# Kernel optimization log

Hardware: AMD Instinct MI355X
Metric: run time of the kernel (lower is better)

The kernel has to match this reference:

```python
import jax, jax.numpy as jnp
import numpy as np

H = 8192  # hidden_size == input_size
NNZ = 1_000_000
B = 128
T = 64


def _spmm(rows, cols, values, x, out_dim):
    # y[r, :] += v * x[c, :] for each nnz (r, c, v); matches coalesced COO spmm
    gathered = values[:, None] * x[cols]          # [nnz, B]
    return jax.ops.segment_sum(gathered, rows, num_segments=out_dim)  # [out_dim, B]


def setup_inputs() -> dict:
    key = jax.random.key(0)
    ks = jax.random.split(key, 5)
    x = jax.random.normal(ks[0], (B, T, H), dtype=jnp.float32)
    ih_indices = jax.random.randint(ks[1], (2, NNZ), 0, H, dtype=jnp.int32)
    hh_indices = jax.random.randint(ks[2], (2, NNZ), 0, H, dtype=jnp.int32)
    # scale so tanh pre-activations stay in a reasonable range (~122 nnz/row)
    ih_values = jax.random.normal(ks[3], (NNZ,), dtype=jnp.float32) * 0.05
    hh_values = jax.random.normal(ks[4], (NNZ,), dtype=jnp.float32) * 0.05
    bias_ih = jnp.zeros((H, 1), dtype=jnp.float32)
    bias_hh = jnp.zeros((H, 1), dtype=jnp.float32)
    return {
        "x": x,
        "ih_indices": ih_indices,
        "ih_values": ih_values,
        "hh_indices": hh_indices,
        "hh_values": hh_values,
        "bias_ih": bias_ih,
        "bias_hh": bias_hh,
    }


def reference(x, ih_indices, ih_values, hh_indices, hh_values, bias_ih, bias_hh):
    # x: (batch, seq, features) -> (T, F, B) as in torch permute(1, 2, 0)
    xs = jnp.transpose(x, (1, 2, 0))  # [T, H, B]
    ih_r, ih_c = ih_indices[0], ih_indices[1]
    hh_r, hh_c = hh_indices[0], hh_indices[1]

    def step(h, x_t):
        pre = (_spmm(ih_r, ih_c, ih_values, x_t, H) + bias_ih
               + _spmm(hh_r, hh_c, hh_values, h, H) + bias_hh)
        h_new = jnp.tanh(pre)
        return h_new, h_new

    h0 = jnp.zeros((H, x.shape[0]), dtype=x.dtype)
    _, out = jax.lax.scan(step, h0, xs)  # out: [T, H, B]
    return jnp.transpose(out, (2, 0, 1))  # [B, T, H] (batch_first)
```

## Files before the change

### kernel.cpp

```cpp
#include <hip/hip_runtime.h>
#include <cstdint>
#include <cstddef>
#include <cstring>

#define H 8192
#define NNZ 1000000
#define B 128
#define T 64

typedef unsigned int u32;
typedef u32 u32x2 __attribute__((ext_vector_type(2)));

__device__ inline float bf_lo(u32 w) { return __uint_as_float(w << 16); }
__device__ inline float bf_hi(u32 w) { return __uint_as_float(w & 0xffff0000u); }
__device__ inline unsigned short f2bf(float f) {
    u32 v = __float_as_uint(f);
    v += 0x7fffu + ((v >> 16) & 1u);
    return (unsigned short)(v >> 16);
}
__device__ inline u32 pack_bf16(float a, float b) {
    return (u32)f2bf(a) | ((u32)f2bf(b) << 16);
}
__device__ inline float fast_tanh(float x) {
    float e = __expf(2.0f * x);
    return 1.0f - 2.0f / (e + 1.0f);
}

__global__ void hist_kernel(const int* __restrict__ rows, int nnz, int* __restrict__ count) {
    int j = blockIdx.x * blockDim.x + threadIdx.x;
    if (j < nnz) atomicAdd(&count[rows[j]], 1);
}

__global__ void scan_kernel(const int* __restrict__ cnt0, int* __restrict__ rp0, int* __restrict__ cur0,
                            const int* __restrict__ cnt1, int* __restrict__ rp1, int* __restrict__ cur1) {
    const int* cnt = (blockIdx.x == 0) ? cnt0 : cnt1;
    int* rp  = (blockIdx.x == 0) ? rp0 : rp1;
    int* cur = (blockIdx.x == 0) ? cur0 : cur1;
    __shared__ int buf[1024];
    __shared__ int carry;
    int tid = threadIdx.x;
    if (tid == 0) carry = 0;
    __syncthreads();
    for (int base = 0; base < H; base += 1024) {
        int v = cnt[base + tid];
        buf[tid] = v;
        __syncthreads();
        for (int off = 1; off < 1024; off <<= 1) {
            int t = (tid >= off) ? buf[tid - off] : 0;
            __syncthreads();
            buf[tid] += t;
            __syncthreads();
        }
        int incl = buf[tid];
        int excl = incl - v;
        int c = carry;
        rp[base + tid]  = c + excl;
        cur[base + tid] = c + excl;
        __syncthreads();
        if (tid == 1023) carry = c + incl;
        __syncthreads();
    }
    if (tid == 0) rp[H] = carry;
}

__global__ void scatter_kernel(const int* __restrict__ rows, const int* __restrict__ cols,
                               const float* __restrict__ vals, int nnz,
                               int* __restrict__ cursor, int2* __restrict__ opair) {
    int j = blockIdx.x * blockDim.x + threadIdx.x;
    if (j < nnz) {
        int r = rows[j];
        int p = atomicAdd(&cursor[r], 1);
        opair[p] = make_int2(cols[j], __float_as_int(vals[j]));
    }
}

__global__ void transpose_bf16_kernel(const float* __restrict__ src, u32* __restrict__ dst) {
    __shared__ float tile[32][33];
    int c0 = blockIdx.x * 32;
    int r0 = blockIdx.y * 32;
    int x = threadIdx.x, y = threadIdx.y;
    #pragma unroll
    for (int i = y; i < 32; i += 8) {
        tile[i][x] = src[(size_t)(r0 + i) * (T * H) + (c0 + x)];
    }
    __syncthreads();
    int tid = y * 32 + x;
    #pragma unroll
    for (int idx = tid; idx < 32 * 16; idx += 256) {
        int row = idx >> 4, w = idx & 15;
        u32 word = pack_bf16(tile[2 * w][row], tile[2 * w + 1][row]);
        dst[(size_t)(c0 + row) * 64 + (r0 >> 1) + w] = word;
    }
}

__global__ void transpose_out_kernel(const u32* __restrict__ src, float* __restrict__ dst) {
    __shared__ u32 tile[32][33];
    int c0 = blockIdx.x * 32;
    int w0 = blockIdx.y * 32;
    int x = threadIdx.x, y = threadIdx.y;
    #pragma unroll
    for (int i = y; i < 32; i += 8) {
        tile[i][x] = src[(size_t)(c0 + i) * 64 + (w0 + x)];
    }
    __syncthreads();
    #pragma unroll
    for (int i = y; i < 64; i += 8) {
        int w = i >> 1;
        u32 word = tile[x][w];
        float val = (i & 1) ? bf_hi(word) : bf_lo(word);
        dst[(size_t)(2 * w0 + i) * (size_t)(T * H) + (c0 + x)] = val;
    }
}

__global__ void __launch_bounds__(64) ih_pre_kernel(
    const int* __restrict__ rp, const int2* __restrict__ pair,
    const u32* __restrict__ xTb, u32* __restrict__ pre,
    const float* __restrict__ bias_ih, const float* __restrict__ bias_hh) {
    int bid = blockIdx.x;
    int xcd = bid & 7;
    int i0  = bid >> 3;
    int t   = (xcd << 3) + (i0 >> 13);
    int r   = i0 & (H - 1);
    int lane = threadIdx.x;
    bool hi = lane >= 32;
    int i = lane & 31;
    const char* __restrict__ xtb = (const char*)(xTb + (size_t)t * H * 64);
    const u32 i8 = (u32)i * 8u;
    float ax = 0.f, ay = 0.f, az = 0.f, aw = 0.f;
    int s = rp[r], e = rp[r + 1];
    int j = s;
    for (; j + 16 <= e; j += 16) {
        int2 q[16];
        #pragma unroll
        for (int u = 0; u < 16; ++u) q[u] = pair[j + u];
        u32x2 g[8];
        #pragma unroll
        for (int u = 0; u < 8; ++u) {
            u32 c = (u32)(hi ? q[2 * u + 1].x : q[2 * u].x);
            g[u] = *(const u32x2*)(xtb + ((c << 8) + i8));
        }
        #pragma unroll
        for (int u = 0; u < 8; ++u) {
            float v = __int_as_float(hi ? q[2 * u + 1].y : q[2 * u].y);
            ax = fmaf(v, bf_lo(g[u].x), ax);
            ay = fmaf(v, bf_hi(g[u].x), ay);
            az = fmaf(v, bf_lo(g[u].y), az);
            aw = fmaf(v, bf_hi(g[u].y), aw);
        }
    }
    for (; j + 2 <= e; j += 2) {
        int2 q0 = pair[j], q1 = pair[j + 1];
        u32 c = (u32)(hi ? q1.x : q0.x);
        u32x2 g = *(const u32x2*)(xtb + ((c << 8) + i8));
        float v = __int_as_float(hi ? q1.y : q0.y);
        ax = fmaf(v, bf_lo(g.x), ax);
        ay = fmaf(v, bf_hi(g.x), ay);
        az = fmaf(v, bf_lo(g.y), az);
        aw = fmaf(v, bf_hi(g.y), aw);
    }
    if (j < e) {
        int2 q0 = pair[j];
        u32 c = (u32)q0.x;
        u32x2 g = *(const u32x2*)(xtb + ((c << 8) + i8));
        float v = hi ? 0.0f : __int_as_float(q0.y);
        ax = fmaf(v, bf_lo(g.x), ax);
        ay = fmaf(v, bf_hi(g.x), ay);
        az = fmaf(v, bf_lo(g.y), az);
        aw = fmaf(v, bf_hi(g.y), aw);
    }
    float tx = ax + __shfl_xor(ax, 32, 64);
    float ty = ay + __shfl_xor(ay, 32, 64);
    float tz = az + __shfl_xor(az, 32, 64);
    float tw = aw + __shfl_xor(aw, 32, 64);
    if (lane < 32) {
        float bias = bias_ih[r] + bias_hh[r];
        u32x2 pw;
        pw.x = pack_bf16(tx + bias, ty + bias);
        pw.y = pack_bf16(tz + bias, tw + bias);
        __builtin_nontemporal_store(pw, (u32x2*)(pre + ((size_t)t * H + r) * 64) + i);
    }
}

__global__ void __launch_bounds__(256) step_kernel(
    const int* __restrict__ rp, const int2* __restrict__ pair,
    const u32* __restrict__ hprev, u32* __restrict__ hout,
    const u32* __restrict__ pre_t) {
    const int tid  = threadIdx.x;
    const int wav  = tid >> 6;
    const int lane = tid & 63;
    const bool hi  = lane >= 32;
    const int i    = lane & 31;
    const u32 i8   = (u32)i * 8u;
    const int r = __builtin_amdgcn_readfirstlane(((int)blockIdx.x << 2) + wav);
    u32x2 pw = __builtin_nontemporal_load((const u32x2*)pre_t + (size_t)r * 32 + i);
    float ax = 0.f, ay = 0.f, az = 0.f, aw = 0.f;
    if (hprev) {
        const char* __restrict__ hpb = (const char*)hprev;
        int s = rp[r], e = rp[r + 1];
        int j = s;
        for (; j + 16 <= e; j += 16) {
            int2 q[16];
            #pragma unroll
            for (int u = 0; u < 16; ++u) q[u] = pair[j + u];
            u32x2 g[8];
            #pragma unroll
            for (int u = 0; u < 8; ++u) {
                u32 c = (u32)(hi ? q[2 * u + 1].x : q[2 * u].x);
                g[u] = *(const u32x2*)(hpb + ((c << 8) + i8));
            }
            #pragma unroll
            for (int u = 0; u < 8; ++u) {
                float v = __int_as_float(hi ? q[2 * u + 1].y : q[2 * u].y);
                ax = fmaf(v, bf_lo(g[u].x), ax);
                ay = fmaf(v, bf_hi(g[u].x), ay);
                az = fmaf(v, bf_lo(g[u].y), az);
                aw = fmaf(v, bf_hi(g[u].y), aw);
            }
        }
        for (; j + 2 <= e; j += 2) {
            int2 q0 = pair[j], q1 = pair[j + 1];
            u32 c = (u32)(hi ? q1.x : q0.x);
            u32x2 g = *(const u32x2*)(hpb + ((c << 8) + i8));
            float v = __int_as_float(hi ? q1.y : q0.y);
            ax = fmaf(v, bf_lo(g.x), ax);
            ay = fmaf(v, bf_hi(g.x), ay);
            az = fmaf(v, bf_lo(g.y), az);
            aw = fmaf(v, bf_hi(g.y), aw);
        }
        if (j < e) {
            int2 q0 = pair[j];
            u32 c = (u32)q0.x;
            u32x2 g = *(const u32x2*)(hpb + ((c << 8) + i8));
            float v = hi ? 0.0f : __int_as_float(q0.y);
            ax = fmaf(v, bf_lo(g.x), ax);
            ay = fmaf(v, bf_hi(g.x), ay);
            az = fmaf(v, bf_lo(g.y), az);
            aw = fmaf(v, bf_hi(g.y), aw);
        }
        ax += __shfl_xor(ax, 32, 64);
        ay += __shfl_xor(ay, 32, 64);
        az += __shfl_xor(az, 32, 64);
        aw += __shfl_xor(aw, 32, 64);
    }
    if (lane < 32) {
        float h0 = fast_tanh(ax + bf_lo(pw.x));
        float h1 = fast_tanh(ay + bf_hi(pw.x));
        float h2v = fast_tanh(az + bf_lo(pw.y));
        float h3 = fast_tanh(aw + bf_hi(pw.y));
        u32x2 hw;
        hw.x = pack_bf16(h0, h1);
        hw.y = pack_bf16(h2v, h3);
        ((u32x2*)hout)[(size_t)r * 32 + i] = hw;
    }
}

extern "C" void kernel_launch(void* const* d_in, const int* in_sizes, int n_in,
                              void* d_out, int out_size, void* d_ws, size_t ws_size,
                              hipStream_t stream) {
    const float* x        = (const float*)d_in[0];
    const int*   ih_idx   = (const int*)d_in[1];
    const float* ih_val   = (const float*)d_in[2];
    const int*   hh_idx   = (const int*)d_in[3];
    const float* hh_val   = (const float*)d_in[4];
    const float* bias_ih  = (const float*)d_in[5];
    const float* bias_hh  = (const float*)d_in[6];
    const int* ih_rows = ih_idx;
    const int* ih_cols = ih_idx + NNZ;
    const int* hh_rows = hh_idx;
    const int* hh_cols = hh_idx + NNZ;

    char* ws = (char*)d_ws;
    size_t off = 0;
    auto alloc = [&](size_t bytes) -> void* {
        void* p = ws + off;
        off += (bytes + 255) & ~(size_t)255;
        return p;
    };
    u32*   xTb     = (u32*)  alloc((size_t)T * H * 64 * 4);
    u32*   pre     = (u32*)  alloc((size_t)T * H * 64 * 4);
    u32*   outb    = (u32*)  alloc((size_t)T * H * 64 * 4);
    int2*  pair_ih = (int2*) alloc((size_t)NNZ * 8);
    int2*  pair_hh = (int2*) alloc((size_t)NNZ * 8);
    int*   rp_ih   = (int*)  alloc((size_t)(H + 1) * 4);
    int*   rp_hh   = (int*)  alloc((size_t)(H + 1) * 4);
    int*   cnt_ih  = (int*)  alloc((size_t)H * 4);
    int*   cnt_hh  = (int*)  alloc((size_t)H * 4);
    int*   cur_ih  = (int*)  alloc((size_t)H * 4);
    int*   cur_hh  = (int*)  alloc((size_t)H * 4);

    hipMemsetAsync(cnt_ih, 0, (size_t)H * 4, stream);
    hipMemsetAsync(cnt_hh, 0, (size_t)H * 4, stream);

    const int tb = 256;
    const int gb = (NNZ + tb - 1) / tb;
    hist_kernel<<<gb, tb, 0, stream>>>(ih_rows, NNZ, cnt_ih);
    hist_kernel<<<gb, tb, 0, stream>>>(hh_rows, NNZ, cnt_hh);
    scan_kernel<<<2, 1024, 0, stream>>>(cnt_ih, rp_ih, cur_ih, cnt_hh, rp_hh, cur_hh);
    scatter_kernel<<<gb, tb, 0, stream>>>(ih_rows, ih_cols, ih_val, NNZ, cur_ih, pair_ih);
    scatter_kernel<<<gb, tb, 0, stream>>>(hh_rows, hh_cols, hh_val, NNZ, cur_hh, pair_hh);

    dim3 tblk(32, 8);
    dim3 tgrid1((T * H) / 32, B / 32);
    transpose_bf16_kernel<<<tgrid1, tblk, 0, stream>>>(x, xTb);

    ih_pre_kernel<<<T * H, 64, 0, stream>>>(rp_ih, pair_ih, xTb, pre, bias_ih, bias_hh);

    step_kernel<<<H / 4, 256, 0, stream>>>(rp_hh, pair_hh, (const u32*)nullptr,
                                           outb, pre);
    for (int t = 1; t < T; ++t) {
        step_kernel<<<H / 4, 256, 0, stream>>>(rp_hh, pair_hh,
                                               outb + (size_t)(t - 1) * H * 64,
                                               outb + (size_t)t * H * 64,
                                               pre + (size_t)t * H * 64);
    }

    dim3 tgrid2((T * H) / 32, 2);
    transpose_out_kernel<<<tgrid2, tblk, 0, stream>>>(outb, (float*)d_out);
}
```

Measured before the change: 2.571 ms.

## Overlap input-projection SpMM with recurrent steps by fusing future timesteps into step kernel

```diff
diff --git a/kernel.cpp b/kernel.cpp
--- a/kernel.cpp
+++ b/kernel.cpp
@@ -26,9 +26,57 @@
     return 1.0f - 2.0f / (e + 1.0f);
 }
 
-__global__ void hist_kernel(const int* __restrict__ rows, int nnz, int* __restrict__ count) {
+__device__ inline void spmm_row(const int* __restrict__ rp, const int2* __restrict__ pair,
+                                const char* __restrict__ basep, int r, bool hi, u32 i8,
+                                float& ax, float& ay, float& az, float& aw) {
+    int s = rp[r], e = rp[r + 1];
+    int j = s;
+    for (; j + 16 <= e; j += 16) {
+        int2 q[16];
+        #pragma unroll
+        for (int u = 0; u < 16; ++u) q[u] = pair[j + u];
+        u32x2 g[8];
+        #pragma unroll
+        for (int u = 0; u < 8; ++u) {
+            u32 c = (u32)(hi ? q[2 * u + 1].x : q[2 * u].x);
+            g[u] = *(const u32x2*)(basep + ((c << 8) + i8));
+        }
+        #pragma unroll
+        for (int u = 0; u < 8; ++u) {
+            float v = __int_as_float(hi ? q[2 * u + 1].y : q[2 * u].y);
+            ax = fmaf(v, bf_lo(g[u].x), ax);
+            ay = fmaf(v, bf_hi(g[u].x), ay);
+            az = fmaf(v, bf_lo(g[u].y), az);
+            aw = fmaf(v, bf_hi(g[u].y), aw);
+        }
+    }
+    for (; j + 2 <= e; j += 2) {
+        int2 q0 = pair[j], q1 = pair[j + 1];
+        u32 c = (u32)(hi ? q1.x : q0.x);
+        u32x2 g = *(const u32x2*)(basep + ((c << 8) + i8));
+        float v = __int_as_float(hi ? q1.y : q0.y);
+        ax = fmaf(v, bf_lo(g.x), ax);
+        ay = fmaf(v, bf_hi(g.x), ay);
+        az = fmaf(v, bf_lo(g.y), az);
+        aw = fmaf(v, bf_hi(g.y), aw);
+    }
+    if (j < e) {
+        int2 q0 = pair[j];
+        u32 c = (u32)q0.x;
+        u32x2 g = *(const u32x2*)(basep + ((c << 8) + i8));
+        float v = hi ? 0.0f : __int_as_float(q0.y);
+        ax = fmaf(v, bf_lo(g.x), ax);
+        ay = fmaf(v, bf_hi(g.x), ay);
+        az = fmaf(v, bf_lo(g.y), az);
+        aw = fmaf(v, bf_hi(g.y), aw);
+    }
+}
+
+__global__ void hist2_kernel(const int* __restrict__ rows_a, const int* __restrict__ rows_b,
+                             int* __restrict__ cnt_a, int* __restrict__ cnt_b) {
     int j = blockIdx.x * blockDim.x + threadIdx.x;
-    if (j < nnz) atomicAdd(&count[rows[j]], 1);
+    if (j < NNZ) atomicAdd(&cnt_a[rows_a[j]], 1);
+    else if (j < 2 * NNZ) atomicAdd(&cnt_b[rows_b[j - NNZ]], 1);
 }
 
 __global__ void scan_kernel(const int* __restrict__ cnt0, int* __restrict__ rp0, int* __restrict__ cur0,
@@ -63,14 +111,22 @@
     if (tid == 0) rp[H] = carry;
 }
 
-__global__ void scatter_kernel(const int* __restrict__ rows, const int* __restrict__ cols,
-                               const float* __restrict__ vals, int nnz,
-                               int* __restrict__ cursor, int2* __restrict__ opair) {
+__global__ void scatter2_kernel(const int* __restrict__ ra, const int* __restrict__ ca,
+                                const float* __restrict__ va, int* __restrict__ cur_a,
+                                int2* __restrict__ pa,
+                                const int* __restrict__ rb, const int* __restrict__ cb,
+                                const float* __restrict__ vb, int* __restrict__ cur_b,
+                                int2* __restrict__ pb) {
     int j = blockIdx.x * blockDim.x + threadIdx.x;
-    if (j < nnz) {
-        int r = rows[j];
-        int p = atomicAdd(&cursor[r], 1);
-        opair[p] = make_int2(cols[j], __float_as_int(vals[j]));
+    if (j < NNZ) {
+        int r = ra[j];
+        int p = atomicAdd(&cur_a[r], 1);
+        pa[p] = make_int2(ca[j], __float_as_int(va[j]));
+    } else if (j < 2 * NNZ) {
+        int jj = j - NNZ;
+        int r = rb[jj];
+        int p = atomicAdd(&cur_b[r], 1);
+        pb[p] = make_int2(cb[jj], __float_as_int(vb[jj]));
     }
 }
 
@@ -112,62 +168,22 @@
     }
 }
 
-__global__ void __launch_bounds__(64) ih_pre_kernel(
+__global__ void __launch_bounds__(256) ih_pre3_kernel(
     const int* __restrict__ rp, const int2* __restrict__ pair,
     const u32* __restrict__ xTb, u32* __restrict__ pre,
     const float* __restrict__ bias_ih, const float* __restrict__ bias_hh) {
-    int bid = blockIdx.x;
-    int xcd = bid & 7;
-    int i0  = bid >> 3;
-    int t   = (xcd << 3) + (i0 >> 13);
-    int r   = i0 & (H - 1);
-    int lane = threadIdx.x;
-    bool hi = lane >= 32;
-    int i = lane & 31;
+    const int tid  = threadIdx.x;
+    const int wav  = tid >> 6;
+    const int lane = tid & 63;
+    const bool hi  = lane >= 32;
+    const int i    = lane & 31;
+    const u32 i8   = (u32)i * 8u;
+    const int w = __builtin_amdgcn_readfirstlane(((int)blockIdx.x << 2) + wav);
+    const int t = w >> 13;
+    const int r = w & (H - 1);
     const char* __restrict__ xtb = (const char*)(xTb + (size_t)t * H * 64);
-    const u32 i8 = (u32)i * 8u;
     float ax = 0.f, ay = 0.f, az = 0.f, aw = 0.f;
-    int s = rp[r], e = rp[r + 1];
-    int j = s;
-    for (; j + 16 <= e; j += 16) {
-        int2 q[16];
-        #pragma unroll
-        for (int u = 0; u < 16; ++u) q[u] = pair[j + u];
-        u32x2 g[8];
-        #pragma unroll
-        for (int u = 0; u < 8; ++u) {
-            u32 c = (u32)(hi ? q[2 * u + 1].x : q[2 * u].x);
-            g[u] = *(const u32x2*)(xtb + ((c << 8) + i8));
-        }
-        #pragma unroll
-        for (int u = 0; u < 8; ++u) {
-            float v = __int_as_float(hi ? q[2 * u + 1].y : q[2 * u].y);
-            ax = fmaf(v, bf_lo(g[u].x), ax);
-            ay = fmaf(v, bf_hi(g[u].x), ay);
-            az = fmaf(v, bf_lo(g[u].y), az);
-            aw = fmaf(v, bf_hi(g[u].y), aw);
-        }
-    }
-    for (; j + 2 <= e; j += 2) {
-        int2 q0 = pair[j], q1 = pair[j + 1];
-        u32 c = (u32)(hi ? q1.x : q0.x);
-        u32x2 g = *(const u32x2*)(xtb + ((c << 8) + i8));
-        float v = __int_as_float(hi ? q1.y : q0.y);
-        ax = fmaf(v, bf_lo(g.x), ax);
-        ay = fmaf(v, bf_hi(g.x), ay);
-        az = fmaf(v, bf_lo(g.y), az);
-        aw = fmaf(v, bf_hi(g.y), aw);
-    }
-    if (j < e) {
-        int2 q0 = pair[j];
-        u32 c = (u32)q0.x;
-        u32x2 g = *(const u32x2*)(xtb + ((c << 8) + i8));
-        float v = hi ? 0.0f : __int_as_float(q0.y);
-        ax = fmaf(v, bf_lo(g.x), ax);
-        ay = fmaf(v, bf_hi(g.x), ay);
-        az = fmaf(v, bf_lo(g.y), az);
-        aw = fmaf(v, bf_hi(g.y), aw);
-    }
+    spmm_row(rp, pair, xtb, r, hi, i8, ax, ay, az, aw);
     float tx = ax + __shfl_xor(ax, 32, 64);
     float ty = ay + __shfl_xor(ay, 32, 64);
     float tz = az + __shfl_xor(az, 32, 64);
@@ -181,76 +197,58 @@
     }
 }
 
-__global__ void __launch_bounds__(256) step_kernel(
-    const int* __restrict__ rp, const int2* __restrict__ pair,
+__global__ void __launch_bounds__(256) fused_step_kernel(
+    const int* __restrict__ rp_hh, const int2* __restrict__ pair_hh,
+    const int* __restrict__ rp_ih, const int2* __restrict__ pair_ih,
+    const u32* __restrict__ xTb, u32* __restrict__ pre,
     const u32* __restrict__ hprev, u32* __restrict__ hout,
-    const u32* __restrict__ pre_t) {
+    const u32* __restrict__ pre_t,
+    const float* __restrict__ bias_ih, const float* __restrict__ bias_hh,
+    int tpre) {
     const int tid  = threadIdx.x;
     const int wav  = tid >> 6;
     const int lane = tid & 63;
     const bool hi  = lane >= 32;
     const int i    = lane & 31;
     const u32 i8   = (u32)i * 8u;
-    const int r = __builtin_amdgcn_readfirstlane(((int)blockIdx.x << 2) + wav);
-    u32x2 pw = __builtin_nontemporal_load((const u32x2*)pre_t + (size_t)r * 32 + i);
-    float ax = 0.f, ay = 0.f, az = 0.f, aw = 0.f;
-    if (hprev) {
-        const char* __restrict__ hpb = (const char*)hprev;
-        int s = rp[r], e = rp[r + 1];
-        int j = s;
-        for (; j + 16 <= e; j += 16) {
-            int2 q[16];
-            #pragma unroll
-            for (int u = 0; u < 16; ++u) q[u] = pair[j + u];
-            u32x2 g[8];
-            #pragma unroll
-            for (int u = 0; u < 8; ++u) {
-                u32 c = (u32)(hi ? q[2 * u + 1].x : q[2 * u].x);
-                g[u] = *(const u32x2*)(hpb + ((c << 8) + i8));
-            }
-            #pragma unroll
-            for (int u = 0; u < 8; ++u) {
-                float v = __int_as_float(hi ? q[2 * u + 1].y : q[2 * u].y);
-                ax = fmaf(v, bf_lo(g[u].x), ax);
-                ay = fmaf(v, bf_hi(g[u].x), ay);
-                az = fmaf(v, bf_lo(g[u].y), az);
-                aw = fmaf(v, bf_hi(g[u].y), aw);
-            }
-        }
-        for (; j + 2 <= e; j += 2) {
-            int2 q0 = pair[j], q1 = pair[j + 1];
-            u32 c = (u32)(hi ? q1.x : q0.x);
-            u32x2 g = *(const u32x2*)(hpb + ((c << 8) + i8));
-            float v = __int_as_float(hi ? q1.y : q0.y);
-            ax = fmaf(v, bf_lo(g.x), ax);
-            ay = fmaf(v, bf_hi(g.x), ay);
-            az = fmaf(v, bf_lo(g.y), az);
-            aw = fmaf(v, bf_hi(g.y), aw);
-        }
-        if (j < e) {
-            int2 q0 = pair[j];
-            u32 c = (u32)q0.x;
-            u32x2 g = *(const u32x2*)(hpb + ((c << 8) + i8));
-            float v = hi ? 0.0f : __int_as_float(q0.y);
-            ax = fmaf(v, bf_lo(g.x), ax);
-            ay = fmaf(v, bf_hi(g.x), ay);
-            az = fmaf(v, bf_lo(g.y), az);
-            aw = fmaf(v, bf_hi(g.y), aw);
-        }
-        ax += __shfl_xor(ax, 32, 64);
-        ay += __shfl_xor(ay, 32, 64);
-        az += __shfl_xor(az, 32, 64);
-        aw += __shfl_xor(aw, 32, 64);
-    }
-    if (lane < 32) {
-        float h0 = fast_tanh(ax + bf_lo(pw.x));
-        float h1 = fast_tanh(ay + bf_hi(pw.x));
-        float h2v = fast_tanh(az + bf_lo(pw.y));
-        float h3 = fast_tanh(aw + bf_hi(pw.y));
-        u32x2 hw;
-        hw.x = pack_bf16(h0, h1);
-        hw.y = pack_bf16(h2v, h3);
-        ((u32x2*)hout)[(size_t)r * 32 + i] = hw;
+    const int bid  = (int)blockIdx.x;
+    if (bid < 2048) {
+        const int r = __builtin_amdgcn_readfirstlane((bid << 2) + wav);
+        u32x2 pw = __builtin_nontemporal_load((const u32x2*)pre_t + (size_t)r * 32 + i);
+        float ax = 0.f, ay = 0.f, az = 0.f, aw = 0.f;
+        if (hprev) {
+            spmm_row(rp_hh, pair_hh, (const char*)hprev, r, hi, i8, ax, ay, az, aw);
+            ax += __shfl_xor(ax, 32, 64);
+            ay += __shfl_xor(ay, 32, 64);
+            az += __shfl_xor(az, 32, 64);
+            aw += __shfl_xor(aw, 32, 64);
+        }
+        if (lane < 32) {
+            float h0 = fast_tanh(ax + bf_lo(pw.x));
+            float h1 = fast_tanh(ay + bf_hi(pw.x));
+            float h2v = fast_tanh(az + bf_lo(pw.y));
+            float h3 = fast_tanh(aw + bf_hi(pw.y));
+            u32x2 hw;
+            hw.x = pack_bf16(h0, h1);
+            hw.y = pack_bf16(h2v, h3);
+            ((u32x2*)hout)[(size_t)r * 32 + i] = hw;
+        }
+    } else {
+        const int r = __builtin_amdgcn_readfirstlane(((bid - 2048) << 2) + wav);
+        const char* __restrict__ xtb = (const char*)(xTb + (size_t)tpre * H * 64);
+        float ax = 0.f, ay = 0.f, az = 0.f, aw = 0.f;
+        spmm_row(rp_ih, pair_ih, xtb, r, hi, i8, ax, ay, az, aw);
+        float tx = ax + __shfl_xor(ax, 32, 64);
+        float ty = ay + __shfl_xor(ay, 32, 64);
+        float tz = az + __shfl_xor(az, 32, 64);
+        float tw = aw + __shfl_xor(aw, 32, 64);
+        if (lane < 32) {
+            float bias = bias_ih[r] + bias_hh[r];
+            u32x2 pw;
+            pw.x = pack_bf16(tx + bias, ty + bias);
+            pw.y = pack_bf16(tz + bias, tw + bias);
+            __builtin_nontemporal_store(pw, (u32x2*)(pre + ((size_t)tpre * H + r) * 64) + i);
+        }
     }
 }
 
@@ -292,26 +290,27 @@
     hipMemsetAsync(cnt_hh, 0, (size_t)H * 4, stream);
 
     const int tb = 256;
-    const int gb = (NNZ + tb - 1) / tb;
-    hist_kernel<<<gb, tb, 0, stream>>>(ih_rows, NNZ, cnt_ih);
-    hist_kernel<<<gb, tb, 0, stream>>>(hh_rows, NNZ, cnt_hh);
+    const int gb2 = (2 * NNZ + tb - 1) / tb;
+    hist2_kernel<<<gb2, tb, 0, stream>>>(ih_rows, hh_rows, cnt_ih, cnt_hh);
     scan_kernel<<<2, 1024, 0, stream>>>(cnt_ih, rp_ih, cur_ih, cnt_hh, rp_hh, cur_hh);
-    scatter_kernel<<<gb, tb, 0, stream>>>(ih_rows, ih_cols, ih_val, NNZ, cur_ih, pair_ih);
-    scatter_kernel<<<gb, tb, 0, stream>>>(hh_rows, hh_cols, hh_val, NNZ, cur_hh, pair_hh);
+    scatter2_kernel<<<gb2, tb, 0, stream>>>(ih_rows, ih_cols, ih_val, cur_ih, pair_ih,
+                                            hh_rows, hh_cols, hh_val, cur_hh, pair_hh);
 
     dim3 tblk(32, 8);
     dim3 tgrid1((T * H) / 32, B / 32);
     transpose_bf16_kernel<<<tgrid1, tblk, 0, stream>>>(x, xTb);
 
-    ih_pre_kernel<<<T * H, 64, 0, stream>>>(rp_ih, pair_ih, xTb, pre, bias_ih, bias_hh);
-
-    step_kernel<<<H / 4, 256, 0, stream>>>(rp_hh, pair_hh, (const u32*)nullptr,
-                                           outb, pre);
-    for (int t = 1; t < T; ++t) {
-        step_kernel<<<H / 4, 256, 0, stream>>>(rp_hh, pair_hh,
-                                               outb + (size_t)(t - 1) * H * 64,
-                                               outb + (size_t)t * H * 64,
-                                               pre + (size_t)t * H * 64);
+    ih_pre3_kernel<<<(3 * H) / 4, 256, 0, stream>>>(rp_ih, pair_ih, xTb, pre, bias_ih, bias_hh);
+
+    for (int t = 0; t < T; ++t) {
+        int tpre = (t + 3 < T) ? (t + 3) : -1;
+        int grid = (tpre >= 0) ? 4096 : 2048;
+        fused_step_kernel<<<grid, 256, 0, stream>>>(
+            rp_hh, pair_hh, rp_ih, pair_ih, xTb, pre,
+            (t > 0) ? (outb + (size_t)(t - 1) * H * 64) : (const u32*)nullptr,
+            outb + (size_t)t * H * 64,
+            pre + (size_t)t * H * 64,
+            bias_ih, bias_hh, tpre);
     }
 
     dim3 tgrid2((T * H) / 32, 2);
```

After: 2.640 ms. 1.03x slower.
